# Optimization experiments

Hardware: AMD Instinct MI355X
Metric: run time of the kernel (lower is better)

The kernel has to match this reference:

```python
import jax, jax.numpy as jnp
import numpy as np

ROPE_BASE = 10000.0


def _rope_cos_sin(seq_len, head_dim, dtype=jnp.float32):
    theta = 1.0 / (ROPE_BASE ** (jnp.arange(0, head_dim, 2, dtype=jnp.float32) / head_dim))
    angles = jnp.arange(seq_len, dtype=jnp.float32)[:, None] * theta[None, :]  # [S, hd/2]
    return jnp.cos(angles).astype(dtype), jnp.sin(angles).astype(dtype)


def _apply_rope(x, cos, sin):
    # x: [B, H, S, hd]; cos/sin: [S, hd/2] broadcast over B,H (interleaved pairing)
    x1 = x[..., 0::2]
    x2 = x[..., 1::2]
    c = cos[None, None, :, :]
    s = sin[None, None, :, :]
    y1 = x1 * c - x2 * s
    y2 = x1 * s + x2 * c
    return jnp.stack([y1, y2], axis=-1).reshape(x.shape)


def setup_inputs() -> dict:
    key = jax.random.key(0)
    ks = jax.random.split(key, 5)
    B, S, D = 2, 2048, 1024
    std = 1.0 / np.sqrt(D)
    return {
        "x": jax.random.normal(ks[0], (B, S, D), dtype=jnp.float32),
        "Wq": jax.random.normal(ks[1], (D, D), dtype=jnp.float32) * std,
        "Wk": jax.random.normal(ks[2], (D, D), dtype=jnp.float32) * std,
        "Wv": jax.random.normal(ks[3], (D, D), dtype=jnp.float32) * std,
        "Wo": jax.random.normal(ks[4], (D, D), dtype=jnp.float32) * std,
        "n_heads": 16,
    }


def reference(x, Wq, Wk, Wv, Wo, n_heads):
    B, S, D = x.shape
    H = n_heads
    hd = D // H
    # QKV projections (nn.Linear: x @ W.T), split into heads -> [B, H, S, hd]
    def proj(W):
        return (x @ W.T).reshape(B, S, H, hd).transpose(0, 2, 1, 3)
    q, k, v = proj(Wq), proj(Wk), proj(Wv)
    cos, sin = _rope_cos_sin(S, hd, x.dtype)
    q = _apply_rope(q, cos, sin)
    k = _apply_rope(k, cos, sin)
    # causal scaled dot-product attention
    scale = 1.0 / np.sqrt(hd)
    scores = jnp.einsum('bhqd,bhkd->bhqk', q, k) * scale
    causal = jnp.tril(jnp.ones((S, S), dtype=bool))
    scores = jnp.where(causal[None, None], scores, jnp.finfo(scores.dtype).min)
    attn = jax.nn.softmax(scores, axis=-1)
    out = jnp.einsum('bhqk,bhkd->bhqd', attn, v)  # [B,H,S,hd]
    out = out.transpose(0, 2, 1, 3).reshape(B, S, D)
    return out @ Wo.T
```

## Files before the change

kernel.cpp:

```cpp
#include <hip/hip_runtime.h>
#include <stdint.h>

#define B_  2
#define S_  2048
#define D_  1024
#define H_  16
#define HD_ 64
#define M_  (B_ * S_)
#define XN_ ((size_t)M_ * D_)
#define WN_ ((size_t)D_ * D_)

using bf16x8 = __attribute__((ext_vector_type(8))) short;
using f32x4  = __attribute__((ext_vector_type(4))) float;

__device__ __forceinline__ unsigned short f2bf(float f) {
    union { float f; unsigned u; } v; v.f = f;
    unsigned u = v.u;
    return (unsigned short)((u + 0x7fffu + ((u >> 16) & 1u)) >> 16);
}
__device__ __forceinline__ unsigned short f2bf_trunc(float f) {
    union { float f; unsigned u; } v; v.f = f;
    return (unsigned short)(v.u >> 16);
}

__device__ __forceinline__ void gload_lds16(const unsigned short* g, unsigned short* l) {
    __builtin_amdgcn_global_load_lds((const __attribute__((address_space(1))) void*)g,
                                     (__attribute__((address_space(3))) void*)l, 16, 0, 0);
}

__global__ __launch_bounds__(256) void cvt_kernel(
    const float* __restrict__ x,
    const float* __restrict__ Wq, const float* __restrict__ Wk,
    const float* __restrict__ Wv, const float* __restrict__ Wo,
    unsigned short* __restrict__ xb,
    unsigned short* __restrict__ Wqb, unsigned short* __restrict__ Wkb,
    unsigned short* __restrict__ Wvb, unsigned short* __restrict__ Wob)
{
    size_t i = ((size_t)blockIdx.x * 256 + threadIdx.x) * 8;
    const float* src; unsigned short* dst; size_t off;
    if (i < XN_) { src = x; dst = xb; off = i; }
    else {
        size_t j = i - XN_;
        int w = (int)(j >> 20);
        off = j & (WN_ - 1);
        src = (w == 0) ? Wq : (w == 1) ? Wk : (w == 2) ? Wv : Wo;
        dst = (w == 0) ? Wqb : (w == 1) ? Wkb : (w == 2) ? Wvb : Wob;
    }
    float4 a = *(const float4*)(src + off);
    float4 b = *(const float4*)(src + off + 4);
    bf16x8 o;
    o[0] = (short)f2bf(a.x); o[1] = (short)f2bf(a.y);
    o[2] = (short)f2bf(a.z); o[3] = (short)f2bf(a.w);
    o[4] = (short)f2bf(b.x); o[5] = (short)f2bf(b.y);
    o[6] = (short)f2bf(b.z); o[7] = (short)f2bf(b.w);
    *(bf16x8*)(dst + off) = o;
}

__global__ __launch_bounds__(256, 3) void qkv_rope_kernel(
    const unsigned short* __restrict__ x,
    const unsigned short* __restrict__ Wq,
    const unsigned short* __restrict__ Wk,
    const unsigned short* __restrict__ Wv,
    unsigned short* __restrict__ Qo,
    unsigned short* __restrict__ Ko,
    unsigned short* __restrict__ Vt)
{
    __shared__ unsigned short As[128 * 64];
    __shared__ unsigned short Bs[128 * 64];
    const int which = blockIdx.z;
    const unsigned short* __restrict__ W = (which == 0) ? Wq : (which == 1) ? Wk : Wv;
    const int tid  = threadIdx.x;
    const int lane = tid & 63, wave = tid >> 6;
    const int col  = lane & 15, quad = lane >> 4;
    const int wm = (wave >> 1) * 64, wn = (wave & 1) * 64;
    const int n0 = blockIdx.x * 128, m0 = blockIdx.y * 128;
    const int sr = tid >> 3;
    const int sc = tid & 7;
    const int ssw = ((sc ^ (sr & 7)) * 8);

    f32x4 acc[4][4];
#pragma unroll
    for (int i = 0; i < 4; ++i)
#pragma unroll
        for (int j = 0; j < 4; ++j) acc[i][j] = (f32x4){0.f, 0.f, 0.f, 0.f};

    for (int k0 = 0; k0 < D_; k0 += 64) {
        __syncthreads();
#pragma unroll
        for (int g = 0; g < 4; ++g) {
            gload_lds16(x + (size_t)(m0 + g * 32 + sr) * D_ + k0 + ssw, As + g * 2048 + tid * 8);
            gload_lds16(W + (size_t)(n0 + g * 32 + sr) * D_ + k0 + ssw, Bs + g * 2048 + tid * 8);
        }
        __syncthreads();
#pragma unroll
        for (int kk = 0; kk < 2; ++kk) {
            bf16x8 af[4], bf[4];
#pragma unroll
            for (int i = 0; i < 4; ++i) {
                const int R = wm + i * 16 + col;
                af[i] = *(const bf16x8*)&As[R * 64 + (((kk * 4 + quad) ^ (R & 7)) * 8)];
            }
#pragma unroll
            for (int j = 0; j < 4; ++j) {
                const int R = wn + j * 16 + col;
                bf[j] = *(const bf16x8*)&Bs[R * 64 + (((kk * 4 + quad) ^ (R & 7)) * 8)];
            }
#pragma unroll
            for (int i = 0; i < 4; ++i)
#pragma unroll
                for (int j = 0; j < 4; ++j)
                    acc[i][j] = __builtin_amdgcn_mfma_f32_16x16x32_bf16(af[i], bf[j], acc[i][j], 0, 0, 0);
        }
    }

#pragma unroll
    for (int i = 0; i < 4; ++i) {
        const int mg0    = m0 + wm + i * 16 + quad * 4;
        const int bb     = mg0 >> 11;
        const int s_base = mg0 & (S_ - 1);
#pragma unroll
        for (int j = 0; j < 4; ++j) {
            const int n  = n0 + wn + j * 16 + col;
            const int h  = n >> 6;
            const int dd = n & 63;
            if (which < 2) {
                unsigned short* __restrict__ O = (which == 0) ? Qo : Ko;
                const float theta  = __expf(-0.2878231366242557f * (float)(dd >> 1));
                const float qscale = (which == 0) ? 0.125f : 1.0f;
#pragma unroll
                for (int r = 0; r < 4; ++r) {
                    float v  = acc[i][j][r];
                    float vp = __shfl_xor(v, 1);
                    float ang = theta * (float)(s_base + r);
                    float sn, cs; __sincosf(ang, &sn, &cs);
                    float y = (dd & 1) ? (vp * sn + v * cs) : (v * cs - vp * sn);
                    O[((size_t)(bb * H_ + h) * S_ + s_base + r) * HD_ + dd] = f2bf(y * qscale);
                }
            } else {
                ushort4 pk;
                pk.x = f2bf(acc[i][j][0]); pk.y = f2bf(acc[i][j][1]);
                pk.z = f2bf(acc[i][j][2]); pk.w = f2bf(acc[i][j][3]);
                *(ushort4*)(Vt + ((size_t)(bb * H_ + h) * HD_ + dd) * S_ + s_base) = pk;
            }
        }
    }
}

#define PST 72

__global__ __launch_bounds__(256, 3) void attn_kernel(
    const unsigned short* __restrict__ Q,
    const unsigned short* __restrict__ K,
    const unsigned short* __restrict__ Vt,
    unsigned short* __restrict__ Aout)
{
    __shared__ unsigned short KS[64 * 64];
    __shared__ unsigned short VS[64 * 64];
    __shared__ unsigned short Plds[4][16 * PST];
    const int tid  = threadIdx.x;
    const int lane = tid & 63;
    const int wave = tid >> 6;
    const int col  = lane & 15;
    const int quad = lane >> 4;
    const int id = blockIdx.x;
    const int bh = (id & 7) * 4 + ((id >> 3) & 3);
    const int t_ = 15 - (id >> 5);
    const int q0blk = t_ * 128;
    const int q0w   = q0blk + wave * 32;
    const int b = bh >> 4, h = bh & 15;

    const unsigned short* Qb = Q  + (size_t)bh * S_ * HD_;
    const unsigned short* Kb = K  + (size_t)bh * S_ * HD_;
    const unsigned short* Vb = Vt + (size_t)bh * HD_ * S_;

    const int srow = tid >> 3;
    const int schk = tid & 7;
    const int ssw0 = (schk ^ (srow & 7)) * 8;

    bf16x8 aq[2][2];
#pragma unroll
    for (int st = 0; st < 2; ++st) {
        aq[st][0] = *(const bf16x8*)(Qb + (size_t)(q0w + st * 16 + col) * HD_ + quad * 8);
        aq[st][1] = *(const bf16x8*)(Qb + (size_t)(q0w + st * 16 + col) * HD_ + 32 + quad * 8);
    }

    f32x4 acc[2][5];
#pragma unroll
    for (int st = 0; st < 2; ++st)
#pragma unroll
        for (int t = 0; t < 5; ++t) acc[st][t] = (f32x4){0.f, 0.f, 0.f, 0.f};
    bf16x8 vone;
#pragma unroll
    for (int e = 0; e < 8; ++e) vone[e] = (short)0x3F80;
    const f32x4 z4 = (f32x4){0.f, 0.f, 0.f, 0.f};
    const float MFIX = 12.0f;

    const int nsteps = (q0blk + 128) >> 6;
    for (int s = 0; s < nsteps; ++s) {
        const int j0 = s << 6;
        __syncthreads();
        gload_lds16(Kb + (size_t)(j0 + srow) * HD_ + ssw0,      KS + tid * 8);
        gload_lds16(Kb + (size_t)(j0 + srow + 32) * HD_ + ssw0, KS + 2048 + tid * 8);
        gload_lds16(Vb + (size_t)srow * S_ + j0 + ssw0,         VS + tid * 8);
        gload_lds16(Vb + (size_t)(srow + 32) * S_ + j0 + ssw0,  VS + 2048 + tid * 8);
        __syncthreads();

        f32x4 sc[2][4];
#pragma unroll
        for (int t2 = 0; t2 < 4; ++t2) {
            const int kr = t2 * 16 + col;
            bf16x8 k0 = *(const bf16x8*)&KS[kr * 64 + ((quad ^ (kr & 7)) * 8)];
            bf16x8 k1 = *(const bf16x8*)&KS[kr * 64 + (((4 + quad) ^ (kr & 7)) * 8)];
            sc[0][t2] = __builtin_amdgcn_mfma_f32_16x16x32_bf16(aq[0][0], k0, z4, 0, 0, 0);
            sc[0][t2] = __builtin_amdgcn_mfma_f32_16x16x32_bf16(aq[0][1], k1, sc[0][t2], 0, 0, 0);
            sc[1][t2] = __builtin_amdgcn_mfma_f32_16x16x32_bf16(aq[1][0], k0, z4, 0, 0, 0);
            sc[1][t2] = __builtin_amdgcn_mfma_f32_16x16x32_bf16(aq[1][1], k1, sc[1][t2], 0, 0, 0);
        }
        bf16x8 vf[8];
#pragma unroll
        for (int t = 0; t < 4; ++t) {
            const int dr = t * 16 + col;
            vf[t * 2]     = *(const bf16x8*)&VS[dr * 64 + ((quad ^ (dr & 7)) * 8)];
            vf[t * 2 + 1] = *(const bf16x8*)&VS[dr * 64 + (((4 + quad) ^ (dr & 7)) * 8)];
        }

#pragma unroll
        for (int st = 0; st < 2; ++st) {
            const bool need_mask = (j0 + 63 > q0w + st * 16);
#pragma unroll
            for (int r = 0; r < 4; ++r) {
                const int qrow = q0w + st * 16 + quad * 4 + r;
                float v0 = sc[st][0][r], v1 = sc[st][1][r], v2 = sc[st][2][r], v3 = sc[st][3][r];
                if (need_mask) {
                    if (j0 + col      > qrow) v0 = -1.0e38f;
                    if (j0 + 16 + col > qrow) v1 = -1.0e38f;
                    if (j0 + 32 + col > qrow) v2 = -1.0e38f;
                    if (j0 + 48 + col > qrow) v3 = -1.0e38f;
                }
                const int rb = (quad * 4 + r) * PST;
                Plds[wave][rb + col]      = f2bf_trunc(__expf(v0 - MFIX));
                Plds[wave][rb + 16 + col] = f2bf_trunc(__expf(v1 - MFIX));
                Plds[wave][rb + 32 + col] = f2bf_trunc(__expf(v2 - MFIX));
                Plds[wave][rb + 48 + col] = f2bf_trunc(__expf(v3 - MFIX));
            }
            bf16x8 ap0 = *(const bf16x8*)&Plds[wave][col * PST + quad * 8];
            bf16x8 ap1 = *(const bf16x8*)&Plds[wave][col * PST + 32 + quad * 8];
#pragma unroll
            for (int t = 0; t < 4; ++t) {
                acc[st][t] = __builtin_amdgcn_mfma_f32_16x16x32_bf16(ap0, vf[t * 2], acc[st][t], 0, 0, 0);
                acc[st][t] = __builtin_amdgcn_mfma_f32_16x16x32_bf16(ap1, vf[t * 2 + 1], acc[st][t], 0, 0, 0);
            }
            acc[st][4] = __builtin_amdgcn_mfma_f32_16x16x32_bf16(ap0, vone, acc[st][4], 0, 0, 0);
            acc[st][4] = __builtin_amdgcn_mfma_f32_16x16x32_bf16(ap1, vone, acc[st][4], 0, 0, 0);
        }
    }

#pragma unroll
    for (int st = 0; st < 2; ++st) {
        float inv[4];
#pragma unroll
        for (int r = 0; r < 4; ++r) inv[r] = 1.0f / acc[st][4][r];
#pragma unroll
        for (int t = 0; t < 4; ++t)
#pragma unroll
            for (int r = 0; r < 4; ++r) {
                const int qrow = q0w + st * 16 + quad * 4 + r;
                Aout[(size_t)(b * S_ + qrow) * D_ + h * HD_ + t * 16 + col] =
                    f2bf(acc[st][t][r] * inv[r]);
            }
    }
}

__global__ __launch_bounds__(256, 3) void oproj_kernel(
    const unsigned short* __restrict__ A,
    const unsigned short* __restrict__ Wo,
    float* __restrict__ out)
{
    __shared__ unsigned short As[128 * 64];
    __shared__ unsigned short Bs[128 * 64];
    const int tid  = threadIdx.x;
    const int lane = tid & 63, wave = tid >> 6;
    const int col  = lane & 15, quad = lane >> 4;
    const int wm = (wave >> 1) * 64, wn = (wave & 1) * 64;
    const int n0 = blockIdx.x * 128, m0 = blockIdx.y * 128;
    const int sr = tid >> 3;
    const int sc = tid & 7;
    const int ssw = ((sc ^ (sr & 7)) * 8);

    f32x4 acc[4][4];
#pragma unroll
    for (int i = 0; i < 4; ++i)
#pragma unroll
        for (int j = 0; j < 4; ++j) acc[i][j] = (f32x4){0.f, 0.f, 0.f, 0.f};

    for (int k0 = 0; k0 < D_; k0 += 64) {
        __syncthreads();
#pragma unroll
        for (int g = 0; g < 4; ++g) {
            gload_lds16(A  + (size_t)(m0 + g * 32 + sr) * D_ + k0 + ssw, As + g * 2048 + tid * 8);
            gload_lds16(Wo + (size_t)(n0 + g * 32 + sr) * D_ + k0 + ssw, Bs + g * 2048 + tid * 8);
        }
        __syncthreads();
#pragma unroll
        for (int kk = 0; kk < 2; ++kk) {
            bf16x8 af[4], bf[4];
#pragma unroll
            for (int i = 0; i < 4; ++i) {
                const int R = wm + i * 16 + col;
                af[i] = *(const bf16x8*)&As[R * 64 + (((kk * 4 + quad) ^ (R & 7)) * 8)];
            }
#pragma unroll
            for (int j = 0; j < 4; ++j) {
                const int R = wn + j * 16 + col;
                bf[j] = *(const bf16x8*)&Bs[R * 64 + (((kk * 4 + quad) ^ (R & 7)) * 8)];
            }
#pragma unroll
            for (int i = 0; i < 4; ++i)
#pragma unroll
                for (int j = 0; j < 4; ++j)
                    acc[i][j] = __builtin_amdgcn_mfma_f32_16x16x32_bf16(af[i], bf[j], acc[i][j], 0, 0, 0);
        }
    }
#pragma unroll
    for (int i = 0; i < 4; ++i) {
        const int mg0 = m0 + wm + i * 16 + quad * 4;
#pragma unroll
        for (int j = 0; j < 4; ++j) {
            const int n = n0 + wn + j * 16 + col;
#pragma unroll
            for (int r = 0; r < 4; ++r)
                out[(size_t)(mg0 + r) * D_ + n] = acc[i][j][r];
        }
    }
}

extern "C" void kernel_launch(void* const* d_in, const int* in_sizes, int n_in,
                              void* d_out, int out_size, void* d_ws, size_t ws_size,
                              hipStream_t stream)
{
    const float* x  = (const float*)d_in[0];
    const float* Wq = (const float*)d_in[1];
    const float* Wk = (const float*)d_in[2];
    const float* Wv = (const float*)d_in[3];
    const float* Wo = (const float*)d_in[4];

    unsigned short* xb  = (unsigned short*)d_ws;
    unsigned short* Wqb = xb  + XN_;
    unsigned short* Wkb = Wqb + WN_;
    unsigned short* Wvb = Wkb + WN_;
    unsigned short* Wob = Wvb + WN_;
    unsigned short* Qw  = Wob + WN_;
    unsigned short* Kw  = Qw  + XN_;
    unsigned short* Vtw = Kw  + XN_;
    unsigned short* Aw  = Vtw + XN_;

    const int cvt_blocks = (int)((XN_ + 4 * WN_) / (8 * 256));
    cvt_kernel<<<cvt_blocks, 256, 0, stream>>>(x, Wq, Wk, Wv, Wo, xb, Wqb, Wkb, Wvb, Wob);
    qkv_rope_kernel<<<dim3(D_ / 128, M_ / 128, 3), 256, 0, stream>>>(xb, Wqb, Wkb, Wvb, Qw, Kw, Vtw);
    attn_kernel<<<512, 256, 0, stream>>>(Qw, Kw, Vtw, Aw);
    oproj_kernel<<<dim3(D_ / 128, M_ / 128), 256, 0, stream>>>(Aw, Wob, (float*)d_out);
}
```

Baseline: 185.3 us.

## Split attention KV range across two blocks with paired query tiles and combine pass

Each attention block now processes a balanced pair of query tiles (p and 15-p) and only every other KV tile, with two halves written as unnormalized numerators and denominators to separate buffers. A new combine kernel sums the two partial results and normalizes before the output projection. This is meant to even out causal load imbalance across blocks. In exchange it adds an extra kernel launch, extra global traffic for partial numerators, and rounds the partial numerators to bf16 before they are summed.

```diff
diff --git a/kernel.cpp b/kernel.cpp
--- a/kernel.cpp
+++ b/kernel.cpp
@@ -21,6 +21,10 @@
 __device__ __forceinline__ unsigned short f2bf_trunc(float f) {
     union { float f; unsigned u; } v; v.f = f;
     return (unsigned short)(v.u >> 16);
+}
+__device__ __forceinline__ float bf2f(unsigned short s) {
+    union { unsigned u; float f; } v; v.u = ((unsigned)s) << 16;
+    return v.f;
 }
 
 __device__ __forceinline__ void gload_lds16(const unsigned short* g, unsigned short* l) {
@@ -152,7 +156,10 @@
     const unsigned short* __restrict__ Q,
     const unsigned short* __restrict__ K,
     const unsigned short* __restrict__ Vt,
-    unsigned short* __restrict__ Aout)
+    unsigned short* __restrict__ num0,
+    unsigned short* __restrict__ num1,
+    float* __restrict__ den0,
+    float* __restrict__ den1)
 {
     __shared__ unsigned short KS[64 * 64];
     __shared__ unsigned short VS[64 * 64];
@@ -164,10 +171,13 @@
     const int quad = lane >> 4;
     const int id = blockIdx.x;
     const int bh = (id & 7) * 4 + ((id >> 3) & 3);
-    const int t_ = 15 - (id >> 5);
-    const int q0blk = t_ * 128;
-    const int q0w   = q0blk + wave * 32;
+    const int ph = id >> 5;
+    const int p  = ph & 7;
+    const int hf = ph >> 3;
     const int b = bh >> 4, h = bh & 15;
+
+    unsigned short* __restrict__ nout = hf ? num1 : num0;
+    float*          __restrict__ dout = hf ? den1 : den0;
 
     const unsigned short* Qb = Q  + (size_t)bh * S_ * HD_;
     const unsigned short* Kb = K  + (size_t)bh * S_ * HD_;
@@ -177,98 +187,127 @@
     const int schk = tid & 7;
     const int ssw0 = (schk ^ (srow & 7)) * 8;
 
-    bf16x8 aq[2][2];
-#pragma unroll
-    for (int st = 0; st < 2; ++st) {
-        aq[st][0] = *(const bf16x8*)(Qb + (size_t)(q0w + st * 16 + col) * HD_ + quad * 8);
-        aq[st][1] = *(const bf16x8*)(Qb + (size_t)(q0w + st * 16 + col) * HD_ + 32 + quad * 8);
-    }
-
-    f32x4 acc[2][5];
-#pragma unroll
-    for (int st = 0; st < 2; ++st)
-#pragma unroll
-        for (int t = 0; t < 5; ++t) acc[st][t] = (f32x4){0.f, 0.f, 0.f, 0.f};
     bf16x8 vone;
 #pragma unroll
     for (int e = 0; e < 8; ++e) vone[e] = (short)0x3F80;
     const f32x4 z4 = (f32x4){0.f, 0.f, 0.f, 0.f};
     const float MFIX = 12.0f;
 
-    const int nsteps = (q0blk + 128) >> 6;
-    for (int s = 0; s < nsteps; ++s) {
-        const int j0 = s << 6;
-        __syncthreads();
-        gload_lds16(Kb + (size_t)(j0 + srow) * HD_ + ssw0,      KS + tid * 8);
-        gload_lds16(Kb + (size_t)(j0 + srow + 32) * HD_ + ssw0, KS + 2048 + tid * 8);
-        gload_lds16(Vb + (size_t)srow * S_ + j0 + ssw0,         VS + tid * 8);
-        gload_lds16(Vb + (size_t)(srow + 32) * S_ + j0 + ssw0,  VS + 2048 + tid * 8);
-        __syncthreads();
-
-        f32x4 sc[2][4];
-#pragma unroll
-        for (int t2 = 0; t2 < 4; ++t2) {
-            const int kr = t2 * 16 + col;
-            bf16x8 k0 = *(const bf16x8*)&KS[kr * 64 + ((quad ^ (kr & 7)) * 8)];
-            bf16x8 k1 = *(const bf16x8*)&KS[kr * 64 + (((4 + quad) ^ (kr & 7)) * 8)];
-            sc[0][t2] = __builtin_amdgcn_mfma_f32_16x16x32_bf16(aq[0][0], k0, z4, 0, 0, 0);
-            sc[0][t2] = __builtin_amdgcn_mfma_f32_16x16x32_bf16(aq[0][1], k1, sc[0][t2], 0, 0, 0);
-            sc[1][t2] = __builtin_amdgcn_mfma_f32_16x16x32_bf16(aq[1][0], k0, z4, 0, 0, 0);
-            sc[1][t2] = __builtin_amdgcn_mfma_f32_16x16x32_bf16(aq[1][1], k1, sc[1][t2], 0, 0, 0);
-        }
-        bf16x8 vf[8];
-#pragma unroll
-        for (int t = 0; t < 4; ++t) {
-            const int dr = t * 16 + col;
-            vf[t * 2]     = *(const bf16x8*)&VS[dr * 64 + ((quad ^ (dr & 7)) * 8)];
-            vf[t * 2 + 1] = *(const bf16x8*)&VS[dr * 64 + (((4 + quad) ^ (dr & 7)) * 8)];
-        }
-
+    for (int tt = 0; tt < 2; ++tt) {
+        const int t_ = tt ? (15 - p) : p;
+        const int q0blk = t_ * 128;
+        const int q0w   = q0blk + wave * 32;
+        const int nsteps = (q0blk + 128) >> 6;
+
+        bf16x8 aq[2][2];
 #pragma unroll
         for (int st = 0; st < 2; ++st) {
-            const bool need_mask = (j0 + 63 > q0w + st * 16);
-#pragma unroll
-            for (int r = 0; r < 4; ++r) {
-                const int qrow = q0w + st * 16 + quad * 4 + r;
-                float v0 = sc[st][0][r], v1 = sc[st][1][r], v2 = sc[st][2][r], v3 = sc[st][3][r];
-                if (need_mask) {
-                    if (j0 + col      > qrow) v0 = -1.0e38f;
-                    if (j0 + 16 + col > qrow) v1 = -1.0e38f;
-                    if (j0 + 32 + col > qrow) v2 = -1.0e38f;
-                    if (j0 + 48 + col > qrow) v3 = -1.0e38f;
+            aq[st][0] = *(const bf16x8*)(Qb + (size_t)(q0w + st * 16 + col) * HD_ + quad * 8);
+            aq[st][1] = *(const bf16x8*)(Qb + (size_t)(q0w + st * 16 + col) * HD_ + 32 + quad * 8);
+        }
+        f32x4 acc[2][5];
+#pragma unroll
+        for (int st = 0; st < 2; ++st)
+#pragma unroll
+            for (int t = 0; t < 5; ++t) acc[st][t] = (f32x4){0.f, 0.f, 0.f, 0.f};
+
+        for (int s = hf; s < nsteps; s += 2) {
+            const int j0 = s << 6;
+            __syncthreads();
+            gload_lds16(Kb + (size_t)(j0 + srow) * HD_ + ssw0,      KS + tid * 8);
+            gload_lds16(Kb + (size_t)(j0 + srow + 32) * HD_ + ssw0, KS + 2048 + tid * 8);
+            gload_lds16(Vb + (size_t)srow * S_ + j0 + ssw0,         VS + tid * 8);
+            gload_lds16(Vb + (size_t)(srow + 32) * S_ + j0 + ssw0,  VS + 2048 + tid * 8);
+            __syncthreads();
+
+            f32x4 sc[2][4];
+#pragma unroll
+            for (int t2 = 0; t2 < 4; ++t2) {
+                const int kr = t2 * 16 + col;
+                bf16x8 k0 = *(const bf16x8*)&KS[kr * 64 + ((quad ^ (kr & 7)) * 8)];
+                bf16x8 k1 = *(const bf16x8*)&KS[kr * 64 + (((4 + quad) ^ (kr & 7)) * 8)];
+                sc[0][t2] = __builtin_amdgcn_mfma_f32_16x16x32_bf16(aq[0][0], k0, z4, 0, 0, 0);
+                sc[0][t2] = __builtin_amdgcn_mfma_f32_16x16x32_bf16(aq[0][1], k1, sc[0][t2], 0, 0, 0);
+                sc[1][t2] = __builtin_amdgcn_mfma_f32_16x16x32_bf16(aq[1][0], k0, z4, 0, 0, 0);
+                sc[1][t2] = __builtin_amdgcn_mfma_f32_16x16x32_bf16(aq[1][1], k1, sc[1][t2], 0, 0, 0);
+            }
+            bf16x8 vf[8];
+#pragma unroll
+            for (int t = 0; t < 4; ++t) {
+                const int dr = t * 16 + col;
+                vf[t * 2]     = *(const bf16x8*)&VS[dr * 64 + ((quad ^ (dr & 7)) * 8)];
+                vf[t * 2 + 1] = *(const bf16x8*)&VS[dr * 64 + (((4 + quad) ^ (dr & 7)) * 8)];
+            }
+
+#pragma unroll
+            for (int st = 0; st < 2; ++st) {
+                const bool need_mask = (j0 + 63 > q0w + st * 16);
+#pragma unroll
+                for (int r = 0; r < 4; ++r) {
+                    const int qrow = q0w + st * 16 + quad * 4 + r;
+                    float v0 = sc[st][0][r], v1 = sc[st][1][r], v2 = sc[st][2][r], v3 = sc[st][3][r];
+                    if (need_mask) {
+                        if (j0 + col      > qrow) v0 = -1.0e38f;
+                        if (j0 + 16 + col > qrow) v1 = -1.0e38f;
+                        if (j0 + 32 + col > qrow) v2 = -1.0e38f;
+                        if (j0 + 48 + col > qrow) v3 = -1.0e38f;
+                    }
+                    const int rb = (quad * 4 + r) * PST;
+                    Plds[wave][rb + col]      = f2bf_trunc(__expf(v0 - MFIX));
+                    Plds[wave][rb + 16 + col] = f2bf_trunc(__expf(v1 - MFIX));
+                    Plds[wave][rb + 32 + col] = f2bf_trunc(__expf(v2 - MFIX));
+                    Plds[wave][rb + 48 + col] = f2bf_trunc(__expf(v3 - MFIX));
                 }
-                const int rb = (quad * 4 + r) * PST;
-                Plds[wave][rb + col]      = f2bf_trunc(__expf(v0 - MFIX));
-                Plds[wave][rb + 16 + col] = f2bf_trunc(__expf(v1 - MFIX));
-                Plds[wave][rb + 32 + col] = f2bf_trunc(__expf(v2 - MFIX));
-                Plds[wave][rb + 48 + col] = f2bf_trunc(__expf(v3 - MFIX));
-            }
-            bf16x8 ap0 = *(const bf16x8*)&Plds[wave][col * PST + quad * 8];
-            bf16x8 ap1 = *(const bf16x8*)&Plds[wave][col * PST + 32 + quad * 8];
-#pragma unroll
-            for (int t = 0; t < 4; ++t) {
-                acc[st][t] = __builtin_amdgcn_mfma_f32_16x16x32_bf16(ap0, vf[t * 2], acc[st][t], 0, 0, 0);
-                acc[st][t] = __builtin_amdgcn_mfma_f32_16x16x32_bf16(ap1, vf[t * 2 + 1], acc[st][t], 0, 0, 0);
-            }
-            acc[st][4] = __builtin_amdgcn_mfma_f32_16x16x32_bf16(ap0, vone, acc[st][4], 0, 0, 0);
-            acc[st][4] = __builtin_amdgcn_mfma_f32_16x16x32_bf16(ap1, vone, acc[st][4], 0, 0, 0);
-        }
-    }
-
-#pragma unroll
-    for (int st = 0; st < 2; ++st) {
-        float inv[4];
-#pragma unroll
-        for (int r = 0; r < 4; ++r) inv[r] = 1.0f / acc[st][4][r];
-#pragma unroll
-        for (int t = 0; t < 4; ++t)
-#pragma unroll
-            for (int r = 0; r < 4; ++r) {
-                const int qrow = q0w + st * 16 + quad * 4 + r;
-                Aout[(size_t)(b * S_ + qrow) * D_ + h * HD_ + t * 16 + col] =
-                    f2bf(acc[st][t][r] * inv[r]);
-            }
-    }
+                bf16x8 ap0 = *(const bf16x8*)&Plds[wave][col * PST + quad * 8];
+                bf16x8 ap1 = *(const bf16x8*)&Plds[wave][col * PST + 32 + quad * 8];
+#pragma unroll
+                for (int t = 0; t < 4; ++t) {
+                    acc[st][t] = __builtin_amdgcn_mfma_f32_16x16x32_bf16(ap0, vf[t * 2], acc[st][t], 0, 0, 0);
+                    acc[st][t] = __builtin_amdgcn_mfma_f32_16x16x32_bf16(ap1, vf[t * 2 + 1], acc[st][t], 0, 0, 0);
+                }
+                acc[st][4] = __builtin_amdgcn_mfma_f32_16x16x32_bf16(ap0, vone, acc[st][4], 0, 0, 0);
+                acc[st][4] = __builtin_amdgcn_mfma_f32_16x16x32_bf16(ap1, vone, acc[st][4], 0, 0, 0);
+            }
+        }
+
+#pragma unroll
+        for (int st = 0; st < 2; ++st) {
+#pragma unroll
+            for (int t = 0; t < 4; ++t)
+#pragma unroll
+                for (int r = 0; r < 4; ++r) {
+                    const int qrow = q0w + st * 16 + quad * 4 + r;
+                    nout[(size_t)(b * S_ + qrow) * D_ + h * HD_ + t * 16 + col] =
+                        f2bf(acc[st][t][r]);
+                }
+            if (col == 0) {
+#pragma unroll
+                for (int r = 0; r < 4; ++r) {
+                    const int qrow = q0w + st * 16 + quad * 4 + r;
+                    dout[(size_t)(b * S_ + qrow) * H_ + h] = acc[st][4][r];
+                }
+            }
+        }
+    }
+}
+
+__global__ __launch_bounds__(256) void combine_kernel(
+    const unsigned short* __restrict__ num0,
+    unsigned short* __restrict__ A,
+    const float* __restrict__ den0,
+    const float* __restrict__ den1)
+{
+    size_t idx = ((size_t)blockIdx.x * 256 + threadIdx.x) * 8;
+    size_t row = idx >> 10;
+    int hh = (int)((idx >> 6) & 15);
+    float inv = 1.0f / (den0[row * H_ + hh] + den1[row * H_ + hh]);
+    bf16x8 a = *(const bf16x8*)(num0 + idx);
+    bf16x8 c = *(const bf16x8*)(A + idx);
+    bf16x8 o;
+#pragma unroll
+    for (int e = 0; e < 8; ++e)
+        o[e] = (short)f2bf((bf2f((unsigned short)a[e]) + bf2f((unsigned short)c[e])) * inv);
+    *(bf16x8*)(A + idx) = o;
 }
 
 __global__ __launch_bounds__(256, 3) void oproj_kernel(
@@ -354,9 +393,14 @@
     unsigned short* Vtw = Kw  + XN_;
     unsigned short* Aw  = Vtw + XN_;
 
+    unsigned short* num0 = xb;
+    float*          den0 = (float*)Wqb;
+    float*          den1 = den0 + (size_t)M_ * H_;
+
     const int cvt_blocks = (int)((XN_ + 4 * WN_) / (8 * 256));
     cvt_kernel<<<cvt_blocks, 256, 0, stream>>>(x, Wq, Wk, Wv, Wo, xb, Wqb, Wkb, Wvb, Wob);
     qkv_rope_kernel<<<dim3(D_ / 128, M_ / 128, 3), 256, 0, stream>>>(xb, Wqb, Wkb, Wvb, Qw, Kw, Vtw);
-    attn_kernel<<<512, 256, 0, stream>>>(Qw, Kw, Vtw, Aw);
+    attn_kernel<<<512, 256, 0, stream>>>(Qw, Kw, Vtw, num0, Aw, den0, den1);
+    combine_kernel<<<(int)(XN_ / (8 * 256)), 256, 0, stream>>>(num0, Aw, den0, den1);
     oproj_kernel<<<dim3(D_ / 128, M_ / 128), 256, 0, stream>>>(Aw, Wob, (float*)d_out);
 }
```

Measured after the change: 172.6 us. 1.07x faster.
